# Kernel tuning notes

Hardware: AMD Instinct MI355X
Metric: run time of the kernel (lower is better)

## Reference

```python
import jax, jax.numpy as jnp
import numpy as np
from jax import lax

# ---- hyperparameters from opt ----
CONV_SIZE = 5          # box-blur kernel size
SQRT_FRAGS = 8         # h/sqrt_frags = patch size (non-overlapping unfold)
TH1_INIT = 0.5         # initial threshold (carried across fragments, as in torch)
PATCH_MEAN = 0.1       # target fraction of on-pixels per fragment
MORPH = 5              # morphology (max/min pool) window, stride 1, pad MORPH//2
TOL = 0.02
STEP = 0.0005

H = W = 4096


def setup_inputs() -> dict:
    key = jax.random.key(0)
    x = jax.random.uniform(key, (1, 1, H, W), dtype=jnp.float32)  # image in [0,1]
    blur_k = jnp.full((1, 1, CONV_SIZE, CONV_SIZE), 1.0 / CONV_SIZE ** 2,
                      dtype=jnp.float32)  # box filter, matches torch.full(...)
    return {"x": x, "blur_k": blur_k}


def _threshold_patches(patches):
    """Sequential per-fragment threshold bisection, th carried across fragments
    exactly like the torch loop mutating self.th1."""
    def frac(patch, t):  # mean of where(patch > t, 1, 0)
        return jnp.mean((patch > t).astype(jnp.float32))

    def frag_step(th, patch):
        # while mean(threshed) < target + 0.02: th -= 0.0005
        th = lax.while_loop(lambda t: frac(patch, t) < PATCH_MEAN + TOL,
                            lambda t: t - STEP, th)
        # while mean(threshed) > target - 0.02: th += 0.0005
        th = lax.while_loop(lambda t: frac(patch, t) > PATCH_MEAN - TOL,
                            lambda t: t + STEP, th)
        return th, (patch > th).astype(jnp.float32)

    _, threshed = lax.scan(frag_step, jnp.float32(TH1_INIT), patches)
    return threshed  # [SF^2, k, k]


def _morph_pool(x, is_max):
    pad = MORPH // 2
    op = x if is_max else -x
    r = lax.reduce_window(op, -jnp.inf, lax.max,
                          (1, 1, MORPH, MORPH), (1, 1, 1, 1),
                          [(0, 0), (0, 0), (pad, pad), (pad, pad)])
    return r if is_max else -r


def reference(x, blur_k):
    N, c, h, w = x.shape  # N = c = 1
    k = h // SQRT_FRAGS
    # box blur, padding='same'
    conved = lax.conv_general_dilated(x.reshape(-1, 1, h, w), blur_k,
                                      (1, 1), "SAME").reshape(N, c, h, w)
    # F.unfold with kernel=stride=k -> non-overlapping patches, row-major order
    patches = (conved.reshape(SQRT_FRAGS, k, SQRT_FRAGS, k)
               .transpose(0, 2, 1, 3)
               .reshape(SQRT_FRAGS ** 2, k, k))
    threshed = lax.stop_gradient(_threshold_patches(patches))
    # F.fold: inverse of the unfold above
    folded = (threshed.reshape(SQRT_FRAGS, SQRT_FRAGS, k, k)
              .transpose(0, 2, 1, 3)
              .reshape(N, c, h, w))
    # morphological close: max-pool then min-pool (min_pool = -maxpool(-x))
    out = _morph_pool(_morph_pool(folded, True), False)
    return out
```

## Files before the change

kernel.cpp:

```cpp
#include <hip/hip_runtime.h>
#include <stdint.h>

#define HH 4096
#define WW 4096
#define NPIX (HH * WW)
#define NBINS 8192
#define NFRAG 64
#define FRAG_PIX (512 * 512)
#define WPR 64
#define NWORDS (HH * WPR)
#define CAP 4096
#define LCAP 2048

#define RANK_HI 230686u
#define RANK_LO 241172u

typedef unsigned long long u64;

__device__ __forceinline__ int bin_of(float v) {
  int b = (int)(v * 8192.0f);
  if (b < 0) b = 0;
  if (b > NBINS - 1) b = NBINS - 1;
  return b;
}

__device__ __forceinline__ u64 spread4(u64 x) {
  x &= 0xFFFFull;
  x = (x | (x << 24)) & 0x000000FF000000FFull;
  x = (x | (x << 12)) & 0x000F000F000F000Full;
  x = (x | (x << 6))  & 0x0303030303030303ull;
  x = (x | (x << 3))  & 0x1111111111111111ull;
  return x;
}

__device__ __forceinline__ float blur_tree(const float rowbuf[5][8], int e) {
  const float K = (float)(1.0 / 25.0);
  float p[25];
#pragma unroll
  for (int i = 0; i < 25; ++i) {
    p[i] = __fmul_rn(rowbuf[i / 5][e + (i % 5)], K);
  }
  float r0 = __fadd_rn(__fadd_rn(p[0], p[8]),  p[16]);
  float r1 = __fadd_rn(__fadd_rn(p[1], p[9]),  p[17]);
  float r2 = __fadd_rn(__fadd_rn(p[2], p[10]), p[18]);
  float r3 = __fadd_rn(__fadd_rn(p[3], p[11]), p[19]);
  float r4 = __fadd_rn(__fadd_rn(p[4], p[12]), p[20]);
  float r5 = __fadd_rn(__fadd_rn(p[5], p[13]), p[21]);
  float r6 = __fadd_rn(__fadd_rn(p[6], p[14]), p[22]);
  float r7 = __fadd_rn(__fadd_rn(p[7], p[15]), p[23]);
  float res = __fadd_rn(
      __fadd_rn(__fadd_rn(r0, r1), __fadd_rn(r2, r3)),
      __fadd_rn(__fadd_rn(r4, r5), __fadd_rn(r6, r7)));
  return __fadd_rn(res, p[24]);
}

__global__ void __launch_bounds__(512)
blur_hist_kernel(const float* __restrict__ x,
                 float* __restrict__ out,
                 uint32_t* __restrict__ hist) {
  __shared__ uint32_t lh[NBINS];
  int tid = threadIdx.x;
  for (int i = tid; i < NBINS; i += 512) lh[i] = 0;
  __syncthreads();
  int f = blockIdx.x >> 4;
  int s = blockIdx.x & 15;
  int row0 = (f >> 3) * 512 + s * 32;
  int col0 = (f & 7) * 512;
  for (int it = tid; it < 8 * 128; it += 512) {
    int pr = it >> 7;
    int c4 = it & 127;
    int py = row0 + pr * 4;
    int px = col0 + c4 * 4;
    float rb[8][8];
    bool interior = (px >= 2) && (px + 5 < WW);
#pragma unroll
    for (int r = 0; r < 8; ++r) {
      int yy = py - 2 + r;
      if ((unsigned)yy >= (unsigned)HH) {
#pragma unroll
        for (int j = 0; j < 8; ++j) rb[r][j] = 0.0f;
      } else if (interior) {
        const float* rp = x + (size_t)yy * WW + px;
        float2 L = *(const float2*)(rp - 2);
        float4 M = *(const float4*)(rp);
        float2 R = *(const float2*)(rp + 4);
        rb[r][0] = L.x; rb[r][1] = L.y;
        rb[r][2] = M.x; rb[r][3] = M.y;
        rb[r][4] = M.z; rb[r][5] = M.w;
        rb[r][6] = R.x; rb[r][7] = R.y;
      } else {
#pragma unroll
        for (int j = 0; j < 8; ++j) {
          int xx = px - 2 + j;
          rb[r][j] = ((unsigned)xx < (unsigned)WW) ? x[(size_t)yy * WW + xx] : 0.0f;
        }
      }
    }
#pragma unroll
    for (int orow = 0; orow < 4; ++orow) {
      float4 res;
      res.x = blur_tree(rb + orow, 0);
      res.y = blur_tree(rb + orow, 1);
      res.z = blur_tree(rb + orow, 2);
      res.w = blur_tree(rb + orow, 3);
      *(float4*)(out + (size_t)(py + orow) * WW + px) = res;
      atomicAdd(&lh[bin_of(res.x)], 1u);
      atomicAdd(&lh[bin_of(res.y)], 1u);
      atomicAdd(&lh[bin_of(res.z)], 1u);
      atomicAdd(&lh[bin_of(res.w)], 1u);
    }
  }
  __syncthreads();
  uint32_t* hf = hist + f * NBINS;
  int start = ((s << 9) + tid) & (NBINS - 1);
  for (int ii = 0; ii < NBINS; ii += 512) {
    int i = (start + ii) & (NBINS - 1);
    uint32_t c = lh[i];
    if (c) atomicAdd(&hf[i], c);
  }
}

__global__ void __launch_bounds__(256)
findcrit_gather_kernel(const float* __restrict__ blur,
                       const uint32_t* __restrict__ hist,
                       int4* __restrict__ bins4,
                       float* __restrict__ band,
                       uint32_t* __restrict__ bandcnt) {
  __shared__ uint32_t segsum[256];
  __shared__ uint32_t segoff[256];
  __shared__ int4 sres;
  __shared__ float lval[LCAP];
  __shared__ uint32_t lcnt, gbase;
  int f = blockIdx.x >> 4;
  int s = blockIdx.x & 15;
  int tid = threadIdx.x;

  const uint32_t* hf = hist + f * NBINS;
  int base = tid * 32;
  uint32_t h32[32];
  uint32_t sum = 0;
  for (int i = 0; i < 32; ++i) { h32[i] = hf[base + i]; sum += h32[i]; }
  segsum[tid] = sum;
  __syncthreads();
  if (tid == 0) {
    uint32_t a = 0;
    for (int i = 0; i < 256; ++i) { segoff[i] = a; a += segsum[i]; }
  }
  __syncthreads();
  uint32_t st = segoff[tid];
  uint32_t en = st + segsum[tid];
  if (st <= RANK_HI && RANK_HI < en) {
    uint32_t a = st;
    for (int i = 0; i < 32; ++i) {
      uint32_t nx = a + h32[i];
      if (RANK_HI < nx) { sres.x = base + i; sres.z = (int)(RANK_HI - a); break; }
      a = nx;
    }
  }
  if (st <= RANK_LO && RANK_LO < en) {
    uint32_t a = st;
    for (int i = 0; i < 32; ++i) {
      uint32_t nx = a + h32[i];
      if (RANK_LO < nx) { sres.y = base + i; sres.w = (int)(RANK_LO - a); break; }
      a = nx;
    }
  }
  if (tid == 0) lcnt = 0;
  __syncthreads();
  if (s == 0 && tid == 0) bins4[f] = sres;
  int4 info = sres;

  int row0 = (f >> 3) * 512 + s * 32;
  int col0 = (f & 7) * 512;
  for (int it = tid; it < 32 * 128; it += 256) {
    int rr = it >> 7, c4 = it & 127;
    float4 v = *(const float4*)(blur + (size_t)(row0 + rr) * WW + col0 + c4 * 4);
    float vv[4] = {v.x, v.y, v.z, v.w};
#pragma unroll
    for (int e = 0; e < 4; ++e) {
      int b = bin_of(vv[e]);
      if (b == info.x || b == info.y) {
        uint32_t p = atomicAdd(&lcnt, 1u);
        if (p < LCAP) lval[p] = vv[e];
        else {
          uint32_t pos = atomicAdd(&bandcnt[f], 1u);
          if (pos < CAP) band[(size_t)f * CAP + pos] = vv[e];
        }
      }
    }
  }
  __syncthreads();
  uint32_t n = lcnt < LCAP ? lcnt : LCAP;
  if (tid == 0) gbase = atomicAdd(&bandcnt[f], n);
  __syncthreads();
  uint32_t bse = gbase;
  for (uint32_t i = tid; i < n; i += 256) {
    uint32_t pos = bse + i;
    if (pos < CAP) band[(size_t)f * CAP + pos] = lval[i];
  }
}

__global__ void __launch_bounds__(256)
select_walk_kernel(const float* __restrict__ band,
                   const uint32_t* __restrict__ bandcnt,
                   const int4* __restrict__ bins4,
                   float2* __restrict__ vhl,
                   uint32_t* __restrict__ done,
                   float* __restrict__ th_out) {
  __shared__ uint32_t wv[CAP];
  __shared__ uint32_t hist8[256];
  __shared__ uint32_t scan[256];
  __shared__ uint32_t resbits[2];
  __shared__ int kcur;
  __shared__ uint32_t pref;
  __shared__ uint32_t ticket;
  int f = blockIdx.x;
  int tid = threadIdx.x;
  int n = (int)bandcnt[f];
  if (n > CAP) n = CAP;
  for (int i = tid; i < n; i += 256)
    wv[i] = __float_as_uint(band[(size_t)f * CAP + i]);
  __syncthreads();
  int4 info = bins4[f];
#pragma unroll
  for (int sel = 0; sel < 2; ++sel) {
    int tb = sel ? info.y : info.x;
    int ktgt = sel ? info.w : info.z;
    if (tid == 0) { kcur = ktgt; pref = 0u; }
    __syncthreads();
    for (int pass = 0; pass < 4; ++pass) {
      int shift = 24 - pass * 8;
      uint32_t mhi = (pass == 0) ? 0u : (0xFFFFFFFFu << (shift + 8));
      uint32_t want = pref;
      uint32_t kk = (uint32_t)kcur;
      hist8[tid] = 0u;
      __syncthreads();
      for (int i = tid; i < n; i += 256) {
        uint32_t b = wv[i];
        if (bin_of(__uint_as_float(b)) != tb) continue;
        if ((b & mhi) != want) continue;
        atomicAdd(&hist8[(b >> shift) & 255], 1u);
      }
      __syncthreads();
      uint32_t v = hist8[tid];
      scan[tid] = v;
      __syncthreads();
#pragma unroll
      for (int off = 1; off < 256; off <<= 1) {
        uint32_t t = (tid >= off) ? scan[tid - off] : 0u;
        __syncthreads();
        scan[tid] += t;
        __syncthreads();
      }
      uint32_t inc = scan[tid];
      uint32_t exc = inc - v;
      if (v && kk >= exc && kk < inc) {
        kcur = (int)(kk - exc);
        pref = want | ((uint32_t)tid << shift);
      }
      __syncthreads();
    }
    if (tid == 0) resbits[sel] = pref;
    __syncthreads();
  }
  if (tid == 0)
    vhl[f] = make_float2(__uint_as_float(resbits[0]), __uint_as_float(resbits[1]));
  __threadfence();
  if (tid == 0) ticket = atomicAdd(done, 1u);
  __syncthreads();
  if (ticket == NFRAG - 1) {
    __threadfence();
    if (tid < 64) {
      int lane = tid;
      float2 mine = vhl[lane];
      float th = 0.5f;
      for (int ff = 0; ff < NFRAG; ++ff) {
        float VH = __shfl(mine.x, ff);
        float VL = __shfl(mine.y, ff);
        while (th >= VH) {
#pragma unroll
          for (int i = 0; i < 16; ++i) {
            float t2 = __fadd_rn(th, -0.0005f);
            th = (th >= VH) ? t2 : th;
          }
        }
        while (th < VL) {
#pragma unroll
          for (int i = 0; i < 16; ++i) {
            float t2 = __fadd_rn(th, 0.0005f);
            th = (th < VL) ? t2 : th;
          }
        }
        if (lane == 0) th_out[ff] = th;
      }
    }
  }
}

__global__ void __launch_bounds__(256)
mask_pack_kernel(const float* __restrict__ blur,
                 const float* __restrict__ th,
                 u64* __restrict__ pk) {
  int f = blockIdx.x >> 4;
  int s = blockIdx.x & 15;
  int tid = threadIdx.x;
  int lane = tid & 63;
  int row0 = (f >> 3) * 512 + s * 32;
  int col0 = (f & 7) * 512;
  float tf = th[f];
  for (int it = tid; it < 32 * 128; it += 256) {
    int rr = it >> 7, c4 = it & 127;
    float4 v = *(const float4*)(blur + (size_t)(row0 + rr) * WW + col0 + c4 * 4);
    int g = ((row0 + rr) << 10) + (col0 >> 2) + c4;
    u64 b0 = __ballot(v.x > tf);
    u64 b1 = __ballot(v.y > tf);
    u64 b2 = __ballot(v.z > tf);
    u64 b3 = __ballot(v.w > tf);
    if ((lane & 15) == 0) {
      int sh = lane;
      u64 w = spread4(b0 >> sh) | (spread4(b1 >> sh) << 1)
            | (spread4(b2 >> sh) << 2) | (spread4(b3 >> sh) << 3);
      int base_word = ((g - lane) * 4) >> 6;
      pk[base_word + (lane >> 4)] = w;
    }
  }
}

__global__ void __launch_bounds__(256)
morph_kernel(const u64* __restrict__ in, float* __restrict__ out) {
  __shared__ u64 pkin[24][20];
  __shared__ u64 hA[24][20];
  __shared__ u64 nD[20][20];
  __shared__ u64 hB[20][20];
  int bx = blockIdx.x & 3;
  int by = blockIdx.x >> 2;
  int R0 = by * 16, W0 = bx * 16;
  int tid = threadIdx.x;
  for (int it = tid; it < 24 * 20; it += 256) {
    int i = it / 20, j = it % 20;
    int gy = R0 - 4 + i, gx = W0 - 2 + j;
    u64 m = 0;
    if ((unsigned)gy < (unsigned)HH && (unsigned)gx < (unsigned)WPR)
      m = in[gy * WPR + gx];
    pkin[i][j] = m;
  }
  __syncthreads();
  for (int it = tid; it < 24 * 18; it += 256) {
    int i = it / 18, j = 1 + it % 18;
    u64 m = pkin[i][j], l = pkin[i][j - 1], r = pkin[i][j + 1];
    hA[i][j] = m | (m << 1) | (m << 2) | (m >> 1) | (m >> 2)
                 | (l >> 62) | (l >> 63) | (r << 62) | (r << 63);
  }
  __syncthreads();
  for (int it = tid; it < 20 * 18; it += 256) {
    int i = it / 18, j = 1 + it % 18;
    u64 v = hA[i][j] | hA[i + 1][j] | hA[i + 2][j] | hA[i + 3][j] | hA[i + 4][j];
    int gy = R0 - 2 + i, gx = W0 - 2 + j;
    nD[i][j] = ((unsigned)gy < (unsigned)HH && (unsigned)gx < (unsigned)WPR)
                   ? ~v : 0ull;
  }
  __syncthreads();
  for (int it = tid; it < 20 * 16; it += 256) {
    int i = it / 16, j = 2 + it % 16;
    u64 m = nD[i][j], l = nD[i][j - 1], r = nD[i][j + 1];
    hB[i][j] = m | (m << 1) | (m << 2) | (m >> 1) | (m >> 2)
                 | (l >> 62) | (l >> 63) | (r << 62) | (r << 63);
  }
  __syncthreads();
  int colbase = W0 * 64;
  for (int it = tid; it < 16 * 256; it += 256) {
    int o = it >> 8;
    int px0 = (it & 255) * 4;
    int j = 2 + (px0 >> 6);
    u64 v = hB[o][j] | hB[o + 1][j] | hB[o + 2][j] | hB[o + 3][j] | hB[o + 4][j];
    int sh = px0 & 63;
    float4 ov;
    ov.x = (float)(1 - (int)((v >> (sh + 0)) & 1ull));
    ov.y = (float)(1 - (int)((v >> (sh + 1)) & 1ull));
    ov.z = (float)(1 - (int)((v >> (sh + 2)) & 1ull));
    ov.w = (float)(1 - (int)((v >> (sh + 3)) & 1ull));
    *(float4*)(out + (size_t)(R0 + o) * WW + colbase + px0) = ov;
  }
}

extern "C" void kernel_launch(void* const* d_in, const int* in_sizes, int n_in,
                              void* d_out, int out_size, void* d_ws, size_t ws_size,
                              hipStream_t stream) {
  const float* x = (const float*)d_in[0];
  if (n_in > 1 && in_sizes[0] != NPIX) x = (const float*)d_in[1];
  float* out = (float*)d_out;
  char* ws = (char*)d_ws;

  const size_t OFF_HIST = 0;
  const size_t OFF_BCNT = 2097152;
  const size_t OFF_DONE = 2097408;
  const size_t OFF_TH   = 2097416;
  const size_t OFF_PKA  = 2097672;
  const size_t OFF_BINS = 6291968;
  const size_t OFF_VHL  = 6292992;
  const size_t OFF_BAND = 6293504;
  const size_t OFF_BLUR = 8388608;
  const size_t WS_NEED  = OFF_BLUR + (size_t)NPIX * sizeof(float);
  uint32_t* hist    = (uint32_t*)(ws + OFF_HIST);
  uint32_t* bandcnt = (uint32_t*)(ws + OFF_BCNT);
  uint32_t* done    = (uint32_t*)(ws + OFF_DONE);
  float*    th      = (float*)(ws + OFF_TH);
  u64*      PKA     = (u64*)(ws + OFF_PKA);
  int4*     bins4   = (int4*)(ws + OFF_BINS);
  float2*   vhl     = (float2*)(ws + OFF_VHL);
  float*    band    = (float*)(ws + OFF_BAND);

  float* blurred = (ws_size >= WS_NEED) ? (float*)(ws + OFF_BLUR) : out;

  const int TPB = 256;

  hipMemsetAsync(hist, 0,
                 (size_t)NFRAG * NBINS * sizeof(uint32_t) + NFRAG * sizeof(uint32_t) + 8,
                 stream);
  blur_hist_kernel<<<1024, 512, 0, stream>>>(x, blurred, hist);
  findcrit_gather_kernel<<<1024, TPB, 0, stream>>>(blurred, hist, bins4, band, bandcnt);
  select_walk_kernel<<<NFRAG, TPB, 0, stream>>>(band, bandcnt, bins4, vhl, done, th);
  mask_pack_kernel<<<1024, TPB, 0, stream>>>(blurred, th, PKA);
  morph_kernel<<<1024, TPB, 0, stream>>>(PKA, out);
}
```

Before: 255.9 us.

## Stage blur input tile in shared memory and reuse LDS for histogram

```diff
diff --git a/kernel.cpp b/kernel.cpp
--- a/kernel.cpp
+++ b/kernel.cpp
@@ -54,65 +54,83 @@
   return __fadd_rn(res, p[24]);
 }
 
+#define SROWS 20
+#define SCOLS 524
 __global__ void __launch_bounds__(512)
 blur_hist_kernel(const float* __restrict__ x,
                  float* __restrict__ out,
                  uint32_t* __restrict__ hist) {
-  __shared__ uint32_t lh[NBINS];
+  __shared__ float smem[SROWS * SCOLS];
   int tid = threadIdx.x;
-  for (int i = tid; i < NBINS; i += 512) lh[i] = 0;
-  __syncthreads();
-  int f = blockIdx.x >> 4;
-  int s = blockIdx.x & 15;
-  int row0 = (f >> 3) * 512 + s * 32;
+  int f = blockIdx.x >> 5;
+  int s = blockIdx.x & 31;
+  int row0 = (f >> 3) * 512 + s * 16;
   int col0 = (f & 7) * 512;
-  for (int it = tid; it < 8 * 128; it += 512) {
-    int pr = it >> 7;
-    int c4 = it & 127;
-    int py = row0 + pr * 4;
-    int px = col0 + c4 * 4;
-    float rb[8][8];
-    bool interior = (px >= 2) && (px + 5 < WW);
-#pragma unroll
-    for (int r = 0; r < 8; ++r) {
-      int yy = py - 2 + r;
-      if ((unsigned)yy >= (unsigned)HH) {
-#pragma unroll
-        for (int j = 0; j < 8; ++j) rb[r][j] = 0.0f;
-      } else if (interior) {
-        const float* rp = x + (size_t)yy * WW + px;
-        float2 L = *(const float2*)(rp - 2);
-        float4 M = *(const float4*)(rp);
-        float2 R = *(const float2*)(rp + 4);
-        rb[r][0] = L.x; rb[r][1] = L.y;
-        rb[r][2] = M.x; rb[r][3] = M.y;
-        rb[r][4] = M.z; rb[r][5] = M.w;
-        rb[r][6] = R.x; rb[r][7] = R.y;
+
+  for (int idx = tid; idx < SROWS * 131; idx += 512) {
+    int r = idx / 131;
+    int c4 = idx - r * 131;
+    int gy = row0 - 2 + r;
+    int gcol = col0 - 4 + c4 * 4;
+    float4 val = make_float4(0.f, 0.f, 0.f, 0.f);
+    if ((unsigned)gy < (unsigned)HH) {
+      if (gcol >= 0 && gcol + 4 <= WW) {
+        val = *(const float4*)(x + (size_t)gy * WW + gcol);
       } else {
-#pragma unroll
-        for (int j = 0; j < 8; ++j) {
-          int xx = px - 2 + j;
-          rb[r][j] = ((unsigned)xx < (unsigned)WW) ? x[(size_t)yy * WW + xx] : 0.0f;
+        float tmp[4];
+#pragma unroll
+        for (int j = 0; j < 4; ++j) {
+          int xx = gcol + j;
+          tmp[j] = ((unsigned)xx < (unsigned)WW) ? x[(size_t)gy * WW + xx] : 0.0f;
         }
-      }
-    }
-#pragma unroll
-    for (int orow = 0; orow < 4; ++orow) {
-      float4 res;
-      res.x = blur_tree(rb + orow, 0);
-      res.y = blur_tree(rb + orow, 1);
-      res.z = blur_tree(rb + orow, 2);
-      res.w = blur_tree(rb + orow, 3);
-      *(float4*)(out + (size_t)(py + orow) * WW + px) = res;
-      atomicAdd(&lh[bin_of(res.x)], 1u);
-      atomicAdd(&lh[bin_of(res.y)], 1u);
-      atomicAdd(&lh[bin_of(res.z)], 1u);
-      atomicAdd(&lh[bin_of(res.w)], 1u);
-    }
-  }
+        val = make_float4(tmp[0], tmp[1], tmp[2], tmp[3]);
+      }
+    }
+    *(float4*)(smem + r * SCOLS + c4 * 4) = val;
+  }
+  __syncthreads();
+
+  int pr = tid >> 7;
+  int pc = tid & 127;
+  int py = row0 + pr * 4;
+  int px = col0 + pc * 4;
+  int sc = pc * 4;
+  float res[16];
+#pragma unroll
+  for (int orow = 0; orow < 4; ++orow) {
+    float w[5][8];
+#pragma unroll
+    for (int r = 0; r < 5; ++r) {
+      int sr = pr * 4 + orow + r;
+      const float* rp = smem + sr * SCOLS + sc;
+      float4 a = *(const float4*)(rp);
+      float4 b = *(const float4*)(rp + 4);
+      float4 c = *(const float4*)(rp + 8);
+      w[r][0] = a.z; w[r][1] = a.w;
+      w[r][2] = b.x; w[r][3] = b.y; w[r][4] = b.z; w[r][5] = b.w;
+      w[r][6] = c.x; w[r][7] = c.y;
+    }
+    float4 o4;
+    o4.x = blur_tree(w, 0);
+    o4.y = blur_tree(w, 1);
+    o4.z = blur_tree(w, 2);
+    o4.w = blur_tree(w, 3);
+    *(float4*)(out + (size_t)(py + orow) * WW + px) = o4;
+    res[orow * 4 + 0] = o4.x;
+    res[orow * 4 + 1] = o4.y;
+    res[orow * 4 + 2] = o4.z;
+    res[orow * 4 + 3] = o4.w;
+  }
+  __syncthreads();
+
+  uint32_t* lh = (uint32_t*)smem;
+  for (int i = tid; i < NBINS; i += 512) lh[i] = 0u;
+  __syncthreads();
+#pragma unroll
+  for (int k = 0; k < 16; ++k) atomicAdd(&lh[bin_of(res[k])], 1u);
   __syncthreads();
   uint32_t* hf = hist + f * NBINS;
-  int start = ((s << 9) + tid) & (NBINS - 1);
+  int start = ((s << 8) + tid) & (NBINS - 1);
   for (int ii = 0; ii < NBINS; ii += 512) {
     int i = (start + ii) & (NBINS - 1);
     uint32_t c = lh[i];
@@ -417,7 +435,7 @@
   hipMemsetAsync(hist, 0,
                  (size_t)NFRAG * NBINS * sizeof(uint32_t) + NFRAG * sizeof(uint32_t) + 8,
                  stream);
-  blur_hist_kernel<<<1024, 512, 0, stream>>>(x, blurred, hist);
+  blur_hist_kernel<<<2048, 512, 0, stream>>>(x, blurred, hist);
   findcrit_gather_kernel<<<1024, TPB, 0, stream>>>(blurred, hist, bins4, band, bandcnt);
   select_walk_kernel<<<NFRAG, TPB, 0, stream>>>(band, bandcnt, bins4, vhl, done, th);
   mask_pack_kernel<<<1024, TPB, 0, stream>>>(blurred, th, PKA);
```

Measured after the change: 265.8 us. 1.04x slower.
